# Kernel tuning notes

Measured on AMD Instinct MI355X. Metric: run time of the kernel, lower is better.

Reference implementation:

```python
import jax, jax.numpy as jnp
import numpy as np
from jax import lax

B, S, IN, H, C = 128, 128, 512, 256, 256  # batch, num_sentences, word_hidden*2, sentence_hidden, context
BN_EPS = 1e-5


def setup_inputs() -> dict:
    key = jax.random.key(0)
    ks = jax.random.split(key, 16)
    u = lambda k, shape: jax.random.uniform(k, shape, minval=-0.1, maxval=0.1, dtype=jnp.float32)
    return {
        "x": jax.random.normal(ks[0], (B, S, IN), jnp.float32),
        "sent_hidden_stat": jnp.zeros((2, B, H), jnp.float32),  # unused by forward (as in original)
        "num_sentences_lens": jax.random.randint(ks[1], (B,), 1, S + 1),
        # bidirectional GRU weights (PyTorch layout: [3H, in], gate order r,z,n)
        "w_ih_f": u(ks[2], (3 * H, IN)), "w_hh_f": u(ks[3], (3 * H, H)),
        "b_ih_f": u(ks[4], (3 * H,)),   "b_hh_f": u(ks[5], (3 * H,)),
        "w_ih_b": u(ks[6], (3 * H, IN)), "w_hh_b": u(ks[7], (3 * H, H)),
        "b_ih_b": u(ks[8], (3 * H,)),   "b_hh_b": u(ks[9], (3 * H,)),
        # sentence projection Linear(2H -> C)
        "proj_w": u(ks[10], (C, 2 * H)), "proj_b": u(ks[11], (C,)),
        # BatchNorm1d(num_features=S) affine params
        "bn_gamma": jnp.ones((S,), jnp.float32), "bn_beta": jnp.zeros((S,), jnp.float32),
        # sentence context vector [C, 1]
        "context": u(ks[12], (C, 1)),
    }


def _gru_dir(x, w_ih, w_hh, b_ih, b_hh):
    """Single-direction GRU over x: [B, T, IN] -> [B, T, H] (PyTorch GRU math)."""
    Hd = w_hh.shape[1]
    xp = jnp.einsum('bti,gi->tbg', x, w_ih) + b_ih  # [T, B, 3H], input projections precomputed

    def step(h, xpt):
        hp = h @ w_hh.T + b_hh
        xr, xz, xn = jnp.split(xpt, 3, axis=-1)
        hr, hz, hn = jnp.split(hp, 3, axis=-1)
        r = jax.nn.sigmoid(xr + hr)
        z = jax.nn.sigmoid(xz + hz)
        n = jnp.tanh(xn + r * hn)
        h_new = (1.0 - z) * n + z * h
        return h_new, h_new

    h0 = jnp.zeros((x.shape[0], Hd), x.dtype)
    _, ys = lax.scan(step, h0, xp)
    return jnp.swapaxes(ys, 0, 1)  # [B, T, H]


def reference(x, sent_hidden_stat, num_sentences_lens,
              w_ih_f, w_hh_f, b_ih_f, b_hh_f,
              w_ih_b, w_hh_b, b_ih_b, b_hh_b,
              proj_w, proj_b, bn_gamma, bn_beta, context):
    # Bidirectional GRU over sentences
    out_f = _gru_dir(x, w_ih_f, w_hh_f, b_ih_f, b_hh_f)
    out_b = _gru_dir(x[:, ::-1], w_ih_b, w_hh_b, b_ih_b, b_hh_b)[:, ::-1]
    out = jnp.concatenate([out_f, out_b], axis=-1)  # [B, S, 2H]

    # _fetch/get_mask: zero out positions beyond each document's sentence count
    mask = (jnp.arange(out.shape[1])[None, :] < num_sentences_lens[:, None]).astype(out.dtype)
    out = out * mask[:, :, None]

    # projection -> BatchNorm1d(num_features=S, training stats) -> ReLU
    proj = jnp.einsum('bsd,cd->bsc', out, proj_w) + proj_b  # [B, S, C]
    mu = proj.mean(axis=(0, 2), keepdims=True)
    var = jnp.mean((proj - mu) ** 2, axis=(0, 2), keepdims=True)
    bn = (proj - mu) / jnp.sqrt(var + BN_EPS) * bn_gamma[None, :, None] + bn_beta[None, :, None]
    p = jax.nn.relu(bn)

    # additive attention pooling over sentences
    scores = jnp.einsum('bsc,co->bs', p, context)  # [B, S]
    attn = jax.nn.softmax(scores, axis=1)
    return jnp.einsum('bs,bsd->bd', attn, out)  # [B, 2H]
```

## Files before the change

### kernel.cpp

```cpp
#include <hip/hip_runtime.h>
#include <hip/hip_bf16.h>

#define B_   128
#define S_   128
#define IN_  512
#define H_   256
#define G3_  768
#define C_   256
#define D2H_ 512
#define XPAD 20

typedef short bf16x8 __attribute__((ext_vector_type(8)));
typedef float f32x4  __attribute__((ext_vector_type(4)));

static __device__ __forceinline__ short f2bf(float f) {
  unsigned u = __float_as_uint(f);
  return (short)((u + 0x7fffu + ((u >> 16) & 1u)) >> 16);
}
static __device__ __forceinline__ float bf2f(unsigned short v) {
  return __uint_as_float((unsigned)v << 16);
}

static __device__ __forceinline__ void async16(const void* g, const void* l) {
  __builtin_amdgcn_global_load_lds(
      (const __attribute__((address_space(1))) void*)g,
      (__attribute__((address_space(3))) void*)l, 16, 0, 0);
}

__global__ __launch_bounds__(1024) void pack_wn(
    const float* __restrict__ whf, const float* __restrict__ whb,
    unsigned short* __restrict__ wnp)
{
  const int o = blockIdx.x * 1024 + threadIdx.x;
  const int j    = o & 7;
  const int lane = (o >> 3) & 63;
  const int kk   = (o >> 9) & 7;
  const int tt   = (o >> 12) & 1;
  const int wave = (o >> 13) & 7;
  const int dir  = (o >> 16) & 1;
  const float* w = dir ? whb : whf;
  const int row = wave * 32 + tt * 16 + (lane & 15);
  const int k   = kk * 32 + (lane >> 4) * 8 + j;
  wnp[o] = (unsigned short)f2bf(w[(size_t)(2 * H_ + row) * H_ + k]);
}

__global__ __launch_bounds__(256) void xp_gemm_bf(
    const float* __restrict__ x,
    const float* __restrict__ wf, const float* __restrict__ wb,
    const float* __restrict__ bif, const float* __restrict__ bhf,
    const float* __restrict__ bib, const float* __restrict__ bhb,
    unsigned short* __restrict__ xpf, unsigned short* __restrict__ xpb)
{
  const int sb = blockIdx.x;
  const int bn = blockIdx.y;
  const bool fwd = (bn < 6);
  const float* __restrict__ wsrc = fwd ? wf : wb;
  const float* __restrict__ bi   = fwd ? bif : bib;
  const float* __restrict__ bh   = fwd ? bhf : bhb;
  const int nloc0 = (fwd ? bn : bn - 6) * 128;

  __shared__ __align__(16) unsigned short As[128][56];
  __shared__ __align__(16) unsigned short Bs[128][56];

  const int tid  = threadIdx.x;
  const int wave = tid >> 6, lane = tid & 63;
  const int col  = lane & 15, lg = lane >> 4;
  const int wm   = wave >> 1, wn = wave & 1;
  const int rr   = tid >> 1;
  const int hf   = (tid & 1) * 16;

  const float* ax = x    + ((size_t)(rr * 128 + sb) * IN_ + hf);
  const float* bx = wsrc + ((size_t)(nloc0 + rr) * IN_ + hf);

  f32x4 acc[4][4];
#pragma unroll
  for (int i = 0; i < 4; ++i)
#pragma unroll
    for (int j = 0; j < 4; ++j) acc[i][j] = f32x4{0.f, 0.f, 0.f, 0.f};

  for (int k0 = 0; k0 < IN_; k0 += 32) {
    float4 a0 = *(const float4*)(ax + k0);
    float4 a1 = *(const float4*)(ax + k0 + 4);
    float4 a2 = *(const float4*)(ax + k0 + 8);
    float4 a3 = *(const float4*)(ax + k0 + 12);
    float4 c0 = *(const float4*)(bx + k0);
    float4 c1 = *(const float4*)(bx + k0 + 4);
    float4 c2 = *(const float4*)(bx + k0 + 8);
    float4 c3 = *(const float4*)(bx + k0 + 12);
    __syncthreads();
    {
      bf16x8 p0, p1;
      p0[0]=f2bf(a0.x); p0[1]=f2bf(a0.y); p0[2]=f2bf(a0.z); p0[3]=f2bf(a0.w);
      p0[4]=f2bf(a1.x); p0[5]=f2bf(a1.y); p0[6]=f2bf(a1.z); p0[7]=f2bf(a1.w);
      p1[0]=f2bf(a2.x); p1[1]=f2bf(a2.y); p1[2]=f2bf(a2.z); p1[3]=f2bf(a2.w);
      p1[4]=f2bf(a3.x); p1[5]=f2bf(a3.y); p1[6]=f2bf(a3.z); p1[7]=f2bf(a3.w);
      *(bf16x8*)&As[rr][hf]     = p0;
      *(bf16x8*)&As[rr][hf + 8] = p1;
      p0[0]=f2bf(c0.x); p0[1]=f2bf(c0.y); p0[2]=f2bf(c0.z); p0[3]=f2bf(c0.w);
      p0[4]=f2bf(c1.x); p0[5]=f2bf(c1.y); p0[6]=f2bf(c1.z); p0[7]=f2bf(c1.w);
      p1[0]=f2bf(c2.x); p1[1]=f2bf(c2.y); p1[2]=f2bf(c2.z); p1[3]=f2bf(c2.w);
      p1[4]=f2bf(c3.x); p1[5]=f2bf(c3.y); p1[6]=f2bf(c3.z); p1[7]=f2bf(c3.w);
      *(bf16x8*)&Bs[rr][hf]     = p0;
      *(bf16x8*)&Bs[rr][hf + 8] = p1;
    }
    __syncthreads();
    bf16x8 af[4], bfv[4];
#pragma unroll
    for (int mi = 0; mi < 4; ++mi)
      af[mi] = *(const bf16x8*)&As[wm * 64 + mi * 16 + col][lg * 8];
#pragma unroll
    for (int ni = 0; ni < 4; ++ni)
      bfv[ni] = *(const bf16x8*)&Bs[wn * 64 + ni * 16 + col][lg * 8];
#pragma unroll
    for (int mi = 0; mi < 4; ++mi)
#pragma unroll
      for (int ni = 0; ni < 4; ++ni)
        acc[mi][ni] = __builtin_amdgcn_mfma_f32_16x16x32_bf16(af[mi], bfv[ni], acc[mi][ni], 0, 0, 0);
  }

  const int t = fwd ? sb : (S_ - 1 - sb);
  unsigned short* __restrict__ dstbase = fwd ? xpf : xpb;
#pragma unroll
  for (int ni = 0; ni < 4; ++ni) {
    const int g = nloc0 + wn * 64 + ni * 16 + col;
    const float bias = bi[g] + (g < 2 * H_ ? bh[g] : 0.f);
#pragma unroll
    for (int mi = 0; mi < 4; ++mi) {
      const int grp = wm * 4 + mi;
      ushort4 o;
      o.x = (unsigned short)f2bf(acc[mi][ni][0] + bias);
      o.y = (unsigned short)f2bf(acc[mi][ni][1] + bias);
      o.z = (unsigned short)f2bf(acc[mi][ni][2] + bias);
      o.w = (unsigned short)f2bf(acc[mi][ni][3] + bias);
      *(ushort4*)(dstbase + (((size_t)t * 8 + grp) * G3_ + g) * XPAD + lg * 4) = o;
    }
  }
}

__global__ __launch_bounds__(512, 2) void gru_mfma(
    const unsigned short* __restrict__ xpf, const unsigned short* __restrict__ xpb,
    const float* __restrict__ whf, const float* __restrict__ whb,
    const float* __restrict__ bhf, const float* __restrict__ bhb,
    const unsigned short* __restrict__ wnp,
    const int* __restrict__ lens, float* __restrict__ out)
{
  const int dir = blockIdx.x >> 3;
  const int grp = blockIdx.x & 7;
  const int b0  = grp * 16;
  const unsigned short* __restrict__ xp = dir ? xpb : xpf;
  const float* __restrict__ whh = dir ? whb : whf;
  const float* __restrict__ bhh = dir ? bhb : bhf;

  const int tid  = threadIdx.x;
  const int wave = tid >> 6;
  const int lane = tid & 63;
  const int col  = lane & 15;
  const int lg   = lane >> 4;
  const int gb0  = wave * 32 + col;

  __shared__ __align__(16) unsigned short hlds[2][32][16][8];
  __shared__ __align__(16) unsigned short xlds[2][G3_ * XPAD];

  ((int4*)&hlds[0][0][0][0])[tid] = int4{0, 0, 0, 0};

  {
    const unsigned short* base = xp + (size_t)grp * (G3_ * XPAD);
    const char* lb = (const char*)&xlds[0][0];
#pragma unroll
    for (int j = 0; j < 4; ++j) {
      const int c = j * 512 + tid;
      if (c < 1920)
        async16(base + (size_t)c * 8, lb + (size_t)(j * 512 + wave * 64) * 16);
    }
  }

  bf16x8 wrz[2][2][8];
#pragma unroll
  for (int tt = 0; tt < 2; ++tt) {
    const int gbase = gb0 + tt * 16;
#pragma unroll
    for (int g = 0; g < 2; ++g) {
      const float* wrow = whh + (size_t)(g * H_ + gbase) * H_;
#pragma unroll
      for (int kk = 0; kk < 8; ++kk) {
        const float* pw = wrow + kk * 32 + lg * 8;
        float4 w0 = *(const float4*)pw;
        float4 w1 = *(const float4*)(pw + 4);
        bf16x8 f;
        f[0] = f2bf(w0.x); f[1] = f2bf(w0.y); f[2] = f2bf(w0.z); f[3] = f2bf(w0.w);
        f[4] = f2bf(w1.x); f[5] = f2bf(w1.y); f[6] = f2bf(w1.z); f[7] = f2bf(w1.w);
        wrz[tt][g][kk] = f;
      }
    }
  }

  const unsigned short* wnb = wnp + ((size_t)(dir * 8 + wave) << 13) + lane * 8;

  float bhn[2];
  bhn[0] = bhh[2 * H_ + gb0];
  bhn[1] = bhh[2 * H_ + gb0 + 16];

  int len_[4];
#pragma unroll
  for (int i = 0; i < 4; ++i) len_[i] = lens[b0 + lg * 4 + i];

  float hreg[2][4] = {};

  const int s0 = dir ? (S_ - 1) : 0;
  float* op[4];
#pragma unroll
  for (int i = 0; i < 4; ++i)
    op[i] = out + ((size_t)(b0 + lg * 4 + i) * S_ + s0) * D2H_ + dir * H_ + gb0;
  const ptrdiff_t sdelta = dir ? -(ptrdiff_t)D2H_ : (ptrdiff_t)D2H_;

  int p = 0;
  for (int t = 0; t < S_; ++t) {
    __syncthreads();
    const int xb = t & 1;

    bf16x8 wn[2][8];
#pragma unroll
    for (int tt = 0; tt < 2; ++tt)
#pragma unroll
      for (int kk = 0; kk < 8; ++kk)
        wn[tt][kk] = *(const bf16x8*)(wnb + ((tt * 8 + kk) << 9));

    if (t > 0) {
      const int s_prev = dir ? (S_ - t) : (t - 1);
#pragma unroll
      for (int i = 0; i < 4; ++i) {
        const bool m = s_prev < len_[i];
        op[i][0]  = m ? hreg[0][i] : 0.f;
        op[i][16] = m ? hreg[1][i] : 0.f;
        op[i] += sdelta;
      }
    }

    if (t + 1 < S_) {
      const unsigned short* base = xp + ((size_t)(t + 1) * 8 + grp) * (G3_ * XPAD);
      const char* lb = (const char*)&xlds[xb ^ 1][0];
#pragma unroll
      for (int j = 0; j < 4; ++j) {
        const int c = j * 512 + tid;
        if (c < 1920)
          async16(base + (size_t)c * 8, lb + (size_t)(j * 512 + wave * 64) * 16);
      }
    }

#pragma unroll
    for (int tt = 0; tt < 2; ++tt) {
      const int u = gb0 + tt * 16;
      ushort4 r4 = *(const ushort4*)&xlds[xb][(size_t)u * XPAD + lg * 4];
      ushort4 z4 = *(const ushort4*)&xlds[xb][(size_t)(H_ + u) * XPAD + lg * 4];
      f32x4 accr, accz, accn;
      accr[0] = bf2f(r4.x); accr[1] = bf2f(r4.y); accr[2] = bf2f(r4.z); accr[3] = bf2f(r4.w);
      accz[0] = bf2f(z4.x); accz[1] = bf2f(z4.y); accz[2] = bf2f(z4.z); accz[3] = bf2f(z4.w);
      accn = f32x4{bhn[tt], bhn[tt], bhn[tt], bhn[tt]};
#pragma unroll
      for (int kk = 0; kk < 8; ++kk) {
        bf16x8 a = *(const bf16x8*)&hlds[p][kk * 4 + lg][col][0];
        accr = __builtin_amdgcn_mfma_f32_16x16x32_bf16(a, wrz[tt][0][kk], accr, 0, 0, 0);
        accz = __builtin_amdgcn_mfma_f32_16x16x32_bf16(a, wrz[tt][1][kk], accz, 0, 0, 0);
        accn = __builtin_amdgcn_mfma_f32_16x16x32_bf16(a, wn[tt][kk], accn, 0, 0, 0);
      }
      ushort4 n4 = *(const ushort4*)&xlds[xb][(size_t)(2 * H_ + u) * XPAD + lg * 4];
      float hnv[4];
#pragma unroll
      for (int i = 0; i < 4; ++i) {
        float r  = 1.f / (1.f + __expf(-accr[i]));
        float z  = 1.f / (1.f + __expf(-accz[i]));
        float nx = bf2f((&n4.x)[i]) + r * accn[i];
        float n  = 1.f - 2.f / (__expf(2.f * nx) + 1.f);
        float hn = n + z * (hreg[tt][i] - n);
        hreg[tt][i] = hn;
        hnv[i] = hn;
      }
      unsigned pk01, pk23;
      asm("v_cvt_pk_bf16_f32 %0, %1, %2" : "=v"(pk01) : "v"(hnv[0]), "v"(hnv[1]));
      asm("v_cvt_pk_bf16_f32 %0, %1, %2" : "=v"(pk23) : "v"(hnv[2]), "v"(hnv[3]));
      const int kb = u >> 3, jj = u & 7;
      hlds[p ^ 1][kb][lg * 4 + 0][jj] = (unsigned short)(pk01 & 0xffffu);
      hlds[p ^ 1][kb][lg * 4 + 1][jj] = (unsigned short)(pk01 >> 16);
      hlds[p ^ 1][kb][lg * 4 + 2][jj] = (unsigned short)(pk23 & 0xffffu);
      hlds[p ^ 1][kb][lg * 4 + 3][jj] = (unsigned short)(pk23 >> 16);
    }
    p ^= 1;
  }

  {
    const int s_last = dir ? 0 : (S_ - 1);
#pragma unroll
    for (int i = 0; i < 4; ++i) {
      const bool m = s_last < len_[i];
      op[i][0]  = m ? hreg[0][i] : 0.f;
      op[i][16] = m ? hreg[1][i] : 0.f;
    }
  }
}

__global__ __launch_bounds__(256) void proj_gemm(
    const float* __restrict__ a, const float* __restrict__ w,
    const float* __restrict__ bias, float* __restrict__ proj)
{
  const int bm = blockIdx.x;
  const int n0 = blockIdx.y * 64;

  __shared__ float As[16][68];
  __shared__ float Bs[16][68];

  const int tid = threadIdx.x;
  const int row = tid >> 2;
  const int kq  = (tid & 3) << 2;
  const int tx  = tid & 15, ty = tid >> 4;

  const float* arow = a + (size_t)(bm * 64 + row) * D2H_ + kq;
  const float* brow = w + (size_t)(n0 + row) * D2H_ + kq;

  float acc[4][4] = {};

  for (int k0 = 0; k0 < D2H_; k0 += 16) {
    float4 av = *(const float4*)(arow + k0);
    float4 bv = *(const float4*)(brow + k0);
    As[kq + 0][row] = av.x; As[kq + 1][row] = av.y;
    As[kq + 2][row] = av.z; As[kq + 3][row] = av.w;
    Bs[kq + 0][row] = bv.x; Bs[kq + 1][row] = bv.y;
    Bs[kq + 2][row] = bv.z; Bs[kq + 3][row] = bv.w;
    __syncthreads();
#pragma unroll
    for (int k = 0; k < 16; ++k) {
      float4 av2 = *(const float4*)&As[k][ty * 4];
      float4 bv2 = *(const float4*)&Bs[k][tx * 4];
      acc[0][0] += av2.x * bv2.x; acc[0][1] += av2.x * bv2.y; acc[0][2] += av2.x * bv2.z; acc[0][3] += av2.x * bv2.w;
      acc[1][0] += av2.y * bv2.x; acc[1][1] += av2.y * bv2.y; acc[1][2] += av2.y * bv2.z; acc[1][3] += av2.y * bv2.w;
      acc[2][0] += av2.z * bv2.x; acc[2][1] += av2.z * bv2.y; acc[2][2] += av2.z * bv2.z; acc[2][3] += av2.z * bv2.w;
      acc[3][0] += av2.w * bv2.x; acc[3][1] += av2.w * bv2.y; acc[3][2] += av2.w * bv2.z; acc[3][3] += av2.w * bv2.w;
    }
    __syncthreads();
  }

  float4 bv4 = *(const float4*)(bias + n0 + tx * 4);
#pragma unroll
  for (int i = 0; i < 4; ++i) {
    int m = bm * 64 + ty * 4 + i;
    float4 o;
    o.x = acc[i][0] + bv4.x; o.y = acc[i][1] + bv4.y;
    o.z = acc[i][2] + bv4.z; o.w = acc[i][3] + bv4.w;
    *(float4*)(proj + (size_t)m * C_ + n0 + tx * 4) = o;
  }
}

__global__ __launch_bounds__(256) void bn_stats(
    const float* __restrict__ proj, float* __restrict__ mu, float* __restrict__ rstd)
{
  const int s = blockIdx.x, tid = threadIdx.x;
  float sum = 0.f, sq = 0.f;
  for (int b = 0; b < B_; ++b) {
    float v = proj[((size_t)b * S_ + s) * C_ + tid];
    sum += v; sq += v * v;
  }
#pragma unroll
  for (int o = 32; o; o >>= 1) { sum += __shfl_down(sum, o); sq += __shfl_down(sq, o); }
  __shared__ float r1[4], r2[4];
  const int lane = tid & 63, wid = tid >> 6;
  if (!lane) { r1[wid] = sum; r2[wid] = sq; }
  __syncthreads();
  if (!tid) {
    float s1 = r1[0] + r1[1] + r1[2] + r1[3];
    float s2 = r2[0] + r2[1] + r2[2] + r2[3];
    float m = s1 / (float)(B_ * C_);
    float var = s2 / (float)(B_ * C_) - m * m;
    mu[s] = m;
    rstd[s] = rsqrtf(var + 1e-5f);
  }
}

__global__ __launch_bounds__(256) void score_k(
    const float* __restrict__ proj, const float* __restrict__ mu,
    const float* __restrict__ rstd, const float* __restrict__ gamma,
    const float* __restrict__ beta, const float* __restrict__ ctx,
    float* __restrict__ scores)
{
  const int wid = threadIdx.x >> 6, lane = threadIdx.x & 63;
  const int m = blockIdx.x * 4 + wid;
  const int s = m & 127;
  float4 v  = *(const float4*)(proj + (size_t)m * C_ + lane * 4);
  float4 cv = *(const float4*)(ctx + lane * 4);
  const float ms = mu[s], rs = rstd[s], g = gamma[s], be = beta[s];
  float acc = fmaxf((v.x - ms) * rs * g + be, 0.f) * cv.x
            + fmaxf((v.y - ms) * rs * g + be, 0.f) * cv.y
            + fmaxf((v.z - ms) * rs * g + be, 0.f) * cv.z
            + fmaxf((v.w - ms) * rs * g + be, 0.f) * cv.w;
#pragma unroll
  for (int o = 32; o; o >>= 1) acc += __shfl_down(acc, o);
  if (!lane) scores[m] = acc;
}

__global__ __launch_bounds__(128) void softmax_k(
    const float* __restrict__ scores, float* __restrict__ attn)
{
  const int b = blockIdx.x, tid = threadIdx.x;
  float v = scores[b * S_ + tid];
  float mx = v;
#pragma unroll
  for (int o = 32; o; o >>= 1) mx = fmaxf(mx, __shfl_down(mx, o));
  __shared__ float t0[2], t1[2];
  const int lane = tid & 63, wid = tid >> 6;
  if (!lane) t0[wid] = mx;
  __syncthreads();
  mx = fmaxf(t0[0], t0[1]);
  float e = __expf(v - mx);
  float ssum = e;
#pragma unroll
  for (int o = 32; o; o >>= 1) ssum += __shfl_down(ssum, o);
  if (!lane) t1[wid] = ssum;
  __syncthreads();
  attn[b * S_ + tid] = e / (t1[0] + t1[1]);
}

__global__ __launch_bounds__(512) void final_k(
    const float* __restrict__ attn, const float* __restrict__ out,
    float* __restrict__ y)
{
  const int b = blockIdx.x, d = threadIdx.x;
  __shared__ float a[S_];
  if (threadIdx.x < S_) a[threadIdx.x] = attn[b * S_ + threadIdx.x];
  __syncthreads();
  float acc = 0.f;
  for (int s = 0; s < S_; ++s)
    acc += a[s] * out[((size_t)b * S_ + s) * D2H_ + d];
  y[(size_t)b * D2H_ + d] = acc;
}

extern "C" void kernel_launch(void* const* d_in, const int* in_sizes, int n_in,
                              void* d_out, int out_size, void* d_ws, size_t ws_size,
                              hipStream_t stream)
{
  const float* x      = (const float*)d_in[0];
  const int*   lens   = (const int*)d_in[2];
  const float* w_ih_f = (const float*)d_in[3];
  const float* w_hh_f = (const float*)d_in[4];
  const float* b_ih_f = (const float*)d_in[5];
  const float* b_hh_f = (const float*)d_in[6];
  const float* w_ih_b = (const float*)d_in[7];
  const float* w_hh_b = (const float*)d_in[8];
  const float* b_ih_b = (const float*)d_in[9];
  const float* b_hh_b = (const float*)d_in[10];
  const float* proj_w = (const float*)d_in[11];
  const float* proj_b = (const float*)d_in[12];
  const float* gamma  = (const float*)d_in[13];
  const float* beta   = (const float*)d_in[14];
  const float* ctx    = (const float*)d_in[15];

  float* ws = (float*)d_ws;
  float* outm = ws;
  unsigned short* xpf = (unsigned short*)(ws + 8388608);
  unsigned short* xpb = xpf + 15728640;
  unsigned short* wnp = xpb + 15728640;
  float* proj   = ws + 8388608;
  float* mu     = ws + 12582912;
  float* rstd   = ws + 12583040;
  float* scores = ws + 12583168;
  float* attn   = ws + 12599552;

  pack_wn<<<128, 1024, 0, stream>>>(w_hh_f, w_hh_b, wnp);
  xp_gemm_bf<<<dim3(128, 12), 256, 0, stream>>>(
      x, w_ih_f, w_ih_b, b_ih_f, b_hh_f, b_ih_b, b_hh_b, xpf, xpb);
  gru_mfma<<<16, 512, 0, stream>>>(xpf, xpb, w_hh_f, w_hh_b, b_hh_f, b_hh_b,
                                   wnp, lens, outm);
  proj_gemm<<<dim3(256, 4), 256, 0, stream>>>(outm, proj_w, proj_b, proj);
  bn_stats<<<128, 256, 0, stream>>>(proj, mu, rstd);
  score_k<<<4096, 256, 0, stream>>>(proj, mu, rstd, gamma, beta, ctx, scores);
  softmax_k<<<128, 128, 0, stream>>>(scores, attn);
  final_k<<<128, 512, 0, stream>>>(attn, outm, (float*)d_out);
}
```

Measured before the change: 566.6 us.

## Split GRU recurrence into 4-batch blocks across 64 workgroups with packed bf16 weights

The recurrent GRU kernel now runs 64 workgroups of 4 batch rows each instead of 16 workgroups of 16 rows, which spreads the latency-bound sequential loop over more compute units. The 16-wide MFMA tile is padded with zero rows, so only lane group 0 writes outputs and hidden state. The x-projection layout drops the padding and is regrouped into 4-row slices, and all three recurrent gate weights are prepacked to bf16 in one pack kernel rather than converted inside the GRU kernel. Each block still does a full 16-row MFMA per step, so three quarters of the matrix work is wasted, and every block rereads the packed n-gate weights on every step.

After: 460.8 us. 18.7% less time.

```diff
diff --git a/kernel.cpp b/kernel.cpp
--- a/kernel.cpp
+++ b/kernel.cpp
@@ -8,7 +8,6 @@
 #define G3_  768
 #define C_   256
 #define D2H_ 512
-#define XPAD 20
 
 typedef short bf16x8 __attribute__((ext_vector_type(8)));
 typedef float f32x4  __attribute__((ext_vector_type(4)));
@@ -27,21 +26,23 @@
       (__attribute__((address_space(3))) void*)l, 16, 0, 0);
 }
 
-__global__ __launch_bounds__(1024) void pack_wn(
+__global__ __launch_bounds__(1024) void pack_wh(
     const float* __restrict__ whf, const float* __restrict__ whb,
-    unsigned short* __restrict__ wnp)
+    unsigned short* __restrict__ wp)
 {
   const int o = blockIdx.x * 1024 + threadIdx.x;
   const int j    = o & 7;
   const int lane = (o >> 3) & 63;
   const int kk   = (o >> 9) & 7;
   const int tt   = (o >> 12) & 1;
-  const int wave = (o >> 13) & 7;
-  const int dir  = (o >> 16) & 1;
+  const int rest = o >> 13;
+  const int g    = rest % 3;
+  const int wv   = (rest / 3) & 7;
+  const int dir  = rest / 24;
   const float* w = dir ? whb : whf;
-  const int row = wave * 32 + tt * 16 + (lane & 15);
+  const int row = wv * 32 + tt * 16 + (lane & 15);
   const int k   = kk * 32 + (lane >> 4) * 8 + j;
-  wnp[o] = (unsigned short)f2bf(w[(size_t)(2 * H_ + row) * H_ + k]);
+  wp[o] = (unsigned short)f2bf(w[(size_t)(g * H_ + row) * H_ + k]);
 }
 
 __global__ __launch_bounds__(256) void xp_gemm_bf(
@@ -126,29 +127,27 @@
     const float bias = bi[g] + (g < 2 * H_ ? bh[g] : 0.f);
 #pragma unroll
     for (int mi = 0; mi < 4; ++mi) {
-      const int grp = wm * 4 + mi;
+      const int grp = wm * 16 + mi * 4 + lg;
       ushort4 o;
       o.x = (unsigned short)f2bf(acc[mi][ni][0] + bias);
       o.y = (unsigned short)f2bf(acc[mi][ni][1] + bias);
       o.z = (unsigned short)f2bf(acc[mi][ni][2] + bias);
       o.w = (unsigned short)f2bf(acc[mi][ni][3] + bias);
-      *(ushort4*)(dstbase + (((size_t)t * 8 + grp) * G3_ + g) * XPAD + lg * 4) = o;
+      *(ushort4*)(dstbase + (((size_t)t * 32 + grp) * G3_ + g) * 4) = o;
     }
   }
 }
 
 __global__ __launch_bounds__(512, 2) void gru_mfma(
     const unsigned short* __restrict__ xpf, const unsigned short* __restrict__ xpb,
-    const float* __restrict__ whf, const float* __restrict__ whb,
+    const unsigned short* __restrict__ wp,
     const float* __restrict__ bhf, const float* __restrict__ bhb,
-    const unsigned short* __restrict__ wnp,
     const int* __restrict__ lens, float* __restrict__ out)
 {
-  const int dir = blockIdx.x >> 3;
-  const int grp = blockIdx.x & 7;
-  const int b0  = grp * 16;
+  const int dir  = blockIdx.x >> 5;
+  const int grpb = blockIdx.x & 31;
+  const int b0   = grpb * 4;
   const unsigned short* __restrict__ xp = dir ? xpb : xpf;
-  const float* __restrict__ whh = dir ? whb : whf;
   const float* __restrict__ bhh = dir ? bhb : bhf;
 
   const int tid  = threadIdx.x;
@@ -159,42 +158,27 @@
   const int gb0  = wave * 32 + col;
 
   __shared__ __align__(16) unsigned short hlds[2][32][16][8];
-  __shared__ __align__(16) unsigned short xlds[2][G3_ * XPAD];
-
-  ((int4*)&hlds[0][0][0][0])[tid] = int4{0, 0, 0, 0};
+  __shared__ __align__(16) unsigned short xlds[2][G3_ * 4];
+
+  ((int4*)hlds)[tid]       = int4{0, 0, 0, 0};
+  ((int4*)hlds)[512 + tid] = int4{0, 0, 0, 0};
 
   {
-    const unsigned short* base = xp + (size_t)grp * (G3_ * XPAD);
-    const char* lb = (const char*)&xlds[0][0];
-#pragma unroll
-    for (int j = 0; j < 4; ++j) {
-      const int c = j * 512 + tid;
-      if (c < 1920)
-        async16(base + (size_t)c * 8, lb + (size_t)(j * 512 + wave * 64) * 16);
-    }
-  }
+    const unsigned short* base = xp + (size_t)grpb * (G3_ * 4);
+    if (tid < 384)
+      async16(base + (size_t)tid * 8, (const char*)&xlds[0][0] + wave * 1024);
+  }
+
+  const unsigned short* wpb = wp + (size_t)(dir * 8 + wave) * 24576 + lane * 8;
 
   bf16x8 wrz[2][2][8];
 #pragma unroll
-  for (int tt = 0; tt < 2; ++tt) {
-    const int gbase = gb0 + tt * 16;
-#pragma unroll
-    for (int g = 0; g < 2; ++g) {
-      const float* wrow = whh + (size_t)(g * H_ + gbase) * H_;
-#pragma unroll
-      for (int kk = 0; kk < 8; ++kk) {
-        const float* pw = wrow + kk * 32 + lg * 8;
-        float4 w0 = *(const float4*)pw;
-        float4 w1 = *(const float4*)(pw + 4);
-        bf16x8 f;
-        f[0] = f2bf(w0.x); f[1] = f2bf(w0.y); f[2] = f2bf(w0.z); f[3] = f2bf(w0.w);
-        f[4] = f2bf(w1.x); f[5] = f2bf(w1.y); f[6] = f2bf(w1.z); f[7] = f2bf(w1.w);
-        wrz[tt][g][kk] = f;
-      }
-    }
-  }
-
-  const unsigned short* wnb = wnp + ((size_t)(dir * 8 + wave) << 13) + lane * 8;
+  for (int tt = 0; tt < 2; ++tt)
+#pragma unroll
+    for (int g = 0; g < 2; ++g)
+#pragma unroll
+      for (int kk = 0; kk < 8; ++kk)
+        wrz[tt][g][kk] = *(const bf16x8*)(wpb + (((g * 2 + tt) * 8 + kk) << 9));
 
   float bhn[2];
   bhn[0] = bhh[2 * H_ + gb0];
@@ -202,7 +186,7 @@
 
   int len_[4];
 #pragma unroll
-  for (int i = 0; i < 4; ++i) len_[i] = lens[b0 + lg * 4 + i];
+  for (int i = 0; i < 4; ++i) len_[i] = lens[b0 + i];
 
   float hreg[2][4] = {};
 
@@ -210,7 +194,7 @@
   float* op[4];
 #pragma unroll
   for (int i = 0; i < 4; ++i)
-    op[i] = out + ((size_t)(b0 + lg * 4 + i) * S_ + s0) * D2H_ + dir * H_ + gb0;
+    op[i] = out + ((size_t)(b0 + i) * S_ + s0) * D2H_ + dir * H_ + gb0;
   const ptrdiff_t sdelta = dir ? -(ptrdiff_t)D2H_ : (ptrdiff_t)D2H_;
 
   int p = 0;
@@ -223,9 +207,9 @@
     for (int tt = 0; tt < 2; ++tt)
 #pragma unroll
       for (int kk = 0; kk < 8; ++kk)
-        wn[tt][kk] = *(const bf16x8*)(wnb + ((tt * 8 + kk) << 9));
-
-    if (t > 0) {
+        wn[tt][kk] = *(const bf16x8*)(wpb + (((4 + tt) * 8 + kk) << 9));
+
+    if (t > 0 && lg == 0) {
       const int s_prev = dir ? (S_ - t) : (t - 1);
 #pragma unroll
       for (int i = 0; i < 4; ++i) {
@@ -237,21 +221,16 @@
     }
 
     if (t + 1 < S_) {
-      const unsigned short* base = xp + ((size_t)(t + 1) * 8 + grp) * (G3_ * XPAD);
-      const char* lb = (const char*)&xlds[xb ^ 1][0];
-#pragma unroll
-      for (int j = 0; j < 4; ++j) {
-        const int c = j * 512 + tid;
-        if (c < 1920)
-          async16(base + (size_t)c * 8, lb + (size_t)(j * 512 + wave * 64) * 16);
-      }
+      const unsigned short* base = xp + ((size_t)(t + 1) * 32 + grpb) * (G3_ * 4);
+      if (tid < 384)
+        async16(base + (size_t)tid * 8, (const char*)&xlds[xb ^ 1][0] + wave * 1024);
     }
 
 #pragma unroll
     for (int tt = 0; tt < 2; ++tt) {
       const int u = gb0 + tt * 16;
-      ushort4 r4 = *(const ushort4*)&xlds[xb][(size_t)u * XPAD + lg * 4];
-      ushort4 z4 = *(const ushort4*)&xlds[xb][(size_t)(H_ + u) * XPAD + lg * 4];
+      ushort4 r4 = *(const ushort4*)&xlds[xb][u * 4];
+      ushort4 z4 = *(const ushort4*)&xlds[xb][(H_ + u) * 4];
       f32x4 accr, accz, accn;
       accr[0] = bf2f(r4.x); accr[1] = bf2f(r4.y); accr[2] = bf2f(r4.z); accr[3] = bf2f(r4.w);
       accz[0] = bf2f(z4.x); accz[1] = bf2f(z4.y); accz[2] = bf2f(z4.z); accz[3] = bf2f(z4.w);
@@ -263,7 +242,7 @@
         accz = __builtin_amdgcn_mfma_f32_16x16x32_bf16(a, wrz[tt][1][kk], accz, 0, 0, 0);
         accn = __builtin_amdgcn_mfma_f32_16x16x32_bf16(a, wn[tt][kk], accn, 0, 0, 0);
       }
-      ushort4 n4 = *(const ushort4*)&xlds[xb][(size_t)(2 * H_ + u) * XPAD + lg * 4];
+      ushort4 n4 = *(const ushort4*)&xlds[xb][(2 * H_ + u) * 4];
       float hnv[4];
 #pragma unroll
       for (int i = 0; i < 4; ++i) {
@@ -275,19 +254,21 @@
         hreg[tt][i] = hn;
         hnv[i] = hn;
       }
-      unsigned pk01, pk23;
-      asm("v_cvt_pk_bf16_f32 %0, %1, %2" : "=v"(pk01) : "v"(hnv[0]), "v"(hnv[1]));
-      asm("v_cvt_pk_bf16_f32 %0, %1, %2" : "=v"(pk23) : "v"(hnv[2]), "v"(hnv[3]));
-      const int kb = u >> 3, jj = u & 7;
-      hlds[p ^ 1][kb][lg * 4 + 0][jj] = (unsigned short)(pk01 & 0xffffu);
-      hlds[p ^ 1][kb][lg * 4 + 1][jj] = (unsigned short)(pk01 >> 16);
-      hlds[p ^ 1][kb][lg * 4 + 2][jj] = (unsigned short)(pk23 & 0xffffu);
-      hlds[p ^ 1][kb][lg * 4 + 3][jj] = (unsigned short)(pk23 >> 16);
+      if (lg == 0) {
+        unsigned pk01, pk23;
+        asm("v_cvt_pk_bf16_f32 %0, %1, %2" : "=v"(pk01) : "v"(hnv[0]), "v"(hnv[1]));
+        asm("v_cvt_pk_bf16_f32 %0, %1, %2" : "=v"(pk23) : "v"(hnv[2]), "v"(hnv[3]));
+        const int kb = u >> 3, jj = u & 7;
+        hlds[p ^ 1][kb][0][jj] = (unsigned short)(pk01 & 0xffffu);
+        hlds[p ^ 1][kb][1][jj] = (unsigned short)(pk01 >> 16);
+        hlds[p ^ 1][kb][2][jj] = (unsigned short)(pk23 & 0xffffu);
+        hlds[p ^ 1][kb][3][jj] = (unsigned short)(pk23 >> 16);
+      }
     }
     p ^= 1;
   }
 
-  {
+  if (lg == 0) {
     const int s_last = dir ? 0 : (S_ - 1);
 #pragma unroll
     for (int i = 0; i < 4; ++i) {
@@ -454,19 +435,18 @@
   float* ws = (float*)d_ws;
   float* outm = ws;
   unsigned short* xpf = (unsigned short*)(ws + 8388608);
-  unsigned short* xpb = xpf + 15728640;
-  unsigned short* wnp = xpb + 15728640;
+  unsigned short* xpb = xpf + 12582912;
+  unsigned short* wp  = xpb + 12582912;
   float* proj   = ws + 8388608;
   float* mu     = ws + 12582912;
   float* rstd   = ws + 12583040;
   float* scores = ws + 12583168;
   float* attn   = ws + 12599552;
 
-  pack_wn<<<128, 1024, 0, stream>>>(w_hh_f, w_hh_b, wnp);
+  pack_wh<<<384, 1024, 0, stream>>>(w_hh_f, w_hh_b, wp);
   xp_gemm_bf<<<dim3(128, 12), 256, 0, stream>>>(
       x, w_ih_f, w_ih_b, b_ih_f, b_hh_f, b_ih_b, b_hh_b, xpf, xpb);
-  gru_mfma<<<16, 512, 0, stream>>>(xpf, xpb, w_hh_f, w_hh_b, b_hh_f, b_hh_b,
-                                   wnp, lens, outm);
+  gru_mfma<<<64, 512, 0, stream>>>(xpf, xpb, wp, b_hh_f, b_hh_b, lens, outm);
   proj_gemm<<<dim3(256, 4), 256, 0, stream>>>(outm, proj_w, proj_b, proj);
   bn_stats<<<128, 256, 0, stream>>>(proj, mu, rstd);
   score_k<<<4096, 256, 0, stream>>>(proj, mu, rstd, gamma, beta, ctx, scores);
```
